# Kernel tuning notes

Hardware: AMD Instinct MI355X
Metric: run time of the kernel (lower is better)

## Reference

```python
import jax, jax.numpy as jnp
import numpy as np

H = 1024  # hidden_size == input_size


def setup_inputs() -> dict:
    key = jax.random.key(0)
    ks = jax.random.split(key, 12)
    B, T, S, I = 64, 128, 256, 1024
    sc_in = 1.0 / np.sqrt(I)
    sc_h = 1.0 / np.sqrt(H)
    return {
        "trg_emb": jax.random.normal(ks[0], (B, T, I), jnp.float32),
        "h0": jax.random.normal(ks[1], (B, H), jnp.float32),
        "c0": jax.random.normal(ks[2], (B, H), jnp.float32),
        "ctx": jax.random.normal(ks[3], (B, S, H), jnp.float32),
        "src_len": jax.random.randint(ks[4], (B,), 1, S + 1, jnp.int32),
        # nn.LSTM params (gate order i, f, g, o)
        "W_ih": jax.random.uniform(ks[5], (4 * H, I), jnp.float32, -sc_h, sc_h),
        "W_hh": jax.random.uniform(ks[6], (4 * H, H), jnp.float32, -sc_h, sc_h),
        "b_ih": jax.random.uniform(ks[7], (4 * H,), jnp.float32, -sc_h, sc_h),
        "b_hh": jax.random.uniform(ks[8], (4 * H,), jnp.float32, -sc_h, sc_h),
        # GlobalAttention (Luong general): linear_in (H->H), linear_out (2H->H), no bias
        "W_in": jax.random.uniform(ks[9], (H, H), jnp.float32, -sc_h, sc_h),
        "W_out": jax.random.uniform(ks[10], (H, 2 * H), jnp.float32, -sc_h, sc_h),
    }


def _lstm_scan(trg_emb, h0, c0, W_ih, W_hh, b_ih, b_hh):
    # Precompute input contributions for all steps: [B,T,4H] -> scan over T
    x_gates = jnp.einsum('bti,gi->btg', trg_emb, W_ih) + b_ih + b_hh

    def step(carry, xg):
        h, c = carry
        gates = xg + h @ W_hh.T  # [B,4H]
        i, f, g, o = jnp.split(gates, 4, axis=-1)
        c = jax.nn.sigmoid(f) * c + jax.nn.sigmoid(i) * jnp.tanh(g)
        h = jax.nn.sigmoid(o) * jnp.tanh(c)
        return (h, c), h

    (hT, cT), hs = jax.lax.scan(step, (h0, c0), jnp.swapaxes(x_gates, 0, 1))
    return jnp.swapaxes(hs, 0, 1), hT, cT  # [B,T,H], [B,H], [B,H]


def reference(trg_emb, h0, c0, ctx, src_len, W_ih, W_hh, b_ih, b_hh, W_in, W_out):
    # input_feed=False: LSTM recurrence is independent of attention -> run once,
    # then batch the global attention over all T timesteps (same math as the loop).
    lstm_out, hT, cT = _lstm_scan(trg_emb, h0, c0, W_ih, W_hh, b_ih, b_hh)

    q = jnp.einsum('bth,gh->btg', lstm_out, W_in)          # linear_in
    scores = jnp.einsum('bth,bsh->bts', q, ctx)            # [B,T,S]
    mask = jnp.arange(ctx.shape[1])[None, None, :] < src_len[:, None, None]
    scores = jnp.where(mask, scores, -jnp.inf)
    attn = jax.nn.softmax(scores, axis=-1)                 # att_dropout=0
    context = jnp.einsum('bts,bsh->bth', attn, ctx)        # [B,T,H]
    h_tilde = jnp.tanh(
        jnp.einsum('btc,hc->bth', jnp.concatenate([context, lstm_out], axis=-1), W_out)
    )  # [B,T,H]
    return h_tilde, (hT[None], cT[None])
```

## Files before the change

kernel.cpp:

```cpp
#include <hip/hip_runtime.h>
#include <math.h>

#define BB 64
#define TT 128
#define SS 256
#define HHH 1024

typedef unsigned short u16;
typedef unsigned int u32;
typedef unsigned long long u64t;
typedef __bf16 bf16x8 __attribute__((ext_vector_type(8)));
typedef float f32x4 __attribute__((ext_vector_type(4)));
typedef u16 u16x8 __attribute__((ext_vector_type(8)));

__device__ __forceinline__ float sigmoidf_(float x) { return 1.0f / (1.0f + expf(-x)); }
__device__ __forceinline__ u16 f2bf(float f) {
    __bf16 h = (__bf16)f;
    return __builtin_bit_cast(u16, h);
}
__device__ __forceinline__ float b2f(u16 u) {
    return __builtin_bit_cast(float, (u32)u << 16);
}
template <typename OT>
__device__ __forceinline__ void stout(OT* p, float v) {
    if constexpr (sizeof(OT) == 2) *p = f2bf(v); else *p = v;
}
__device__ __forceinline__ void astore(u64t* p, u64t v) {
    __hip_atomic_store(p, v, __ATOMIC_RELAXED, __HIP_MEMORY_SCOPE_AGENT);
}
__device__ __forceinline__ int afetchadd(int* p) {
    return __hip_atomic_fetch_add(p, 1, __ATOMIC_RELAXED, __HIP_MEMORY_SCOPE_AGENT);
}
__device__ __forceinline__ int aload32(const int* p) {
    return __hip_atomic_load(p, __ATOMIC_RELAXED, __HIP_MEMORY_SCOPE_AGENT);
}
__device__ __forceinline__ void astore32(int* p, int v) {
    __hip_atomic_store(p, v, __ATOMIC_RELAXED, __HIP_MEMORY_SCOPE_AGENT);
}
#define GLOAD16(gsrc, ldst)                                                      \
    __builtin_amdgcn_global_load_lds(                                            \
        (const __attribute__((address_space(1))) unsigned int*)(const void*)(gsrc), \
        (__attribute__((address_space(3))) unsigned int*)(void*)(ldst), 16, 0, 0)

__global__ __launch_bounds__(256) void convert_all(
    const float* __restrict__ trg, const float* __restrict__ wih,
    const float* __restrict__ win, const float* __restrict__ wout,
    u16* __restrict__ trg16, u16* __restrict__ wih16,
    u16* __restrict__ win16, u16* __restrict__ wout16)
{
    int b = blockIdx.x;
    const float* in;
    u16* out;
    long base;
    if (b < 4096)      { in = trg;  out = trg16;  base = (long)b * 2048; }
    else if (b < 6144) { in = wih;  out = wih16;  base = (long)(b - 4096) * 2048; }
    else if (b < 6656) { in = win;  out = win16;  base = (long)(b - 6144) * 2048; }
    else               { in = wout; out = wout16; base = (long)(b - 6656) * 2048; }
    long i = base + (long)threadIdx.x * 8;
    float4 a = *(const float4*)(in + i);
    float4 c = *(const float4*)(in + i + 4);
    u16x8 o;
    o[0] = f2bf(a.x); o[1] = f2bf(a.y); o[2] = f2bf(a.z); o[3] = f2bf(a.w);
    o[4] = f2bf(c.x); o[5] = f2bf(c.y); o[6] = f2bf(c.z); o[7] = f2bf(c.w);
    *(u16x8*)(out + i) = o;
}

__global__ __launch_bounds__(128) void wfrag_build(const float* __restrict__ W,
                                                   u16* __restrict__ WF) {
    const int w = blockIdx.x, kq = blockIdx.y, bid = blockIdx.z;
    const int t = threadIdx.x;
    const int rh = t >> 6, lane = t & 63;
    const int rowp = bid * 32 + rh * 16 + (lane & 15);
    const int g = rowp & 3, jrow = rowp >> 2;
    const int k = kq * 256 + w * 32 + (lane >> 4) * 8;
    const float* src = W + ((size_t)(g * 1024 + jrow) << 10) + k;
    float4 v0 = *(const float4*)src;
    float4 v1 = *(const float4*)(src + 4);
    float vv[8] = {v0.x, v0.y, v0.z, v0.w, v1.x, v1.y, v1.z, v1.w};
    u16x8 hi, lo;
#pragma unroll
    for (int i = 0; i < 8; ++i) {
        u16 h = f2bf(vv[i]);
        hi[i] = h;
        lo[i] = f2bf(vv[i] - b2f(h));
    }
    size_t fr = ((((size_t)bid * 4 + kq) * 8 + w) * 2 + rh) * 2;
    *(u16x8*)(WF + fr * 512 + (size_t)lane * 8) = hi;
    *(u16x8*)(WF + (fr + 1) * 512 + (size_t)lane * 8) = lo;
}

__global__ __launch_bounds__(256) void h0frag(const float* __restrict__ h0,
                                              u16* __restrict__ slot) {
    int i = blockIdx.x * 256 + threadIdx.x;
    int b = i >> 7, jg = i & 127;
    int j = jg << 3;
    const float* src = h0 + ((size_t)b << 10) + j;
    float4 v0 = *(const float4*)src;
    float4 v1 = *(const float4*)(src + 4);
    float vv[8] = {v0.x, v0.y, v0.z, v0.w, v1.x, v1.y, v1.z, v1.w};
    u16x8 hi, lo;
#pragma unroll
    for (int e = 0; e < 8; ++e) {
        u16 h = f2bf(vv[e]);
        hi[e] = h;
        lo[e] = f2bf(vv[e] - b2f(h));
    }
    int g = b >> 4, bl = b & 15;
    int kq = j >> 8, w = (j >> 5) & 7, tr = (j >> 3) & 3;
    int lane = tr * 16 + bl;
    size_t base = (size_t)g * 32768 + (size_t)((kq * 8 + w) * 2) * 512 + (size_t)lane * 8;
    *(u16x8*)(slot + base) = hi;
    *(u16x8*)(slot + base + 512) = lo;
}

template <bool TANH, bool AREMAP, bool BIAS, typename OT>
__global__ __launch_bounds__(256) void gemm_mfma_bt(
    const u16* __restrict__ A0, const u16* __restrict__ A1,
    const u16* __restrict__ B, OT* __restrict__ C,
    int M, int N, int K, int KA0,
    const float* __restrict__ bias0, const float* __restrict__ bias1)
{
    __shared__ uint4 As4[512];
    __shared__ uint4 Bs4[512];
    u16* As = (u16*)As4;
    u16* Bs = (u16*)Bs4;
    const int tid = threadIdx.x;
    const int l = tid & 63;
    const int w = tid >> 6;
    const int wm = w >> 1, wn = w & 1;
    const int tc = l & 15, tr8 = (l >> 4) << 3;
    const int m0 = blockIdx.y << 7, n0 = blockIdx.x << 7;
    f32x4 acc[4][4] = {};

    for (int k0 = 0; k0 < K; k0 += 32) {
        const u16* Ap = (k0 < KA0) ? A0 : A1;
        const int koff = (k0 < KA0) ? k0 : k0 - KA0;
#pragma unroll
        for (int r = 0; r < 2; ++r) {
            int u = tid + (r << 8);
            int row = u >> 2, q = u & 3;
            size_t arow;
            if (AREMAP) {
                int rr = m0 + row;
                arow = (size_t)((rr & 63) * 128 + (rr >> 6));
            } else {
                arow = (size_t)(m0 + row);
            }
            GLOAD16(Ap + arow * KA0 + koff + (q << 3), &As4[u]);
            GLOAD16(B + (size_t)(n0 + row) * K + k0 + (q << 3), &Bs4[u]);
        }
        __syncthreads();
        bf16x8 bfr[4];
#pragma unroll
        for (int j = 0; j < 4; ++j)
            bfr[j] = *(const bf16x8*)(Bs + ((wn << 6) + (j << 4) + tc) * 32 + tr8);
#pragma unroll
        for (int i = 0; i < 4; ++i) {
            bf16x8 af = *(const bf16x8*)(As + ((wm << 6) + (i << 4) + tc) * 32 + tr8);
#pragma unroll
            for (int j = 0; j < 4; ++j)
                acc[i][j] = __builtin_amdgcn_mfma_f32_16x16x32_bf16(af, bfr[j], acc[i][j], 0, 0, 0);
        }
        __syncthreads();
    }
#pragma unroll
    for (int j = 0; j < 4; ++j) {
        const int col = n0 + (wn << 6) + (j << 4) + tc;
        const float bias = BIAS ? (bias0[col] + bias1[col]) : 0.0f;
#pragma unroll
        for (int i = 0; i < 4; ++i) {
#pragma unroll
            for (int v = 0; v < 4; ++v) {
                int r = m0 + (wm << 6) + (i << 4) + ((l >> 4) << 2) + v;
                float val = acc[i][j][v] + bias;
                if (TANH) val = tanhf(val);
                stout(&C[(size_t)r * N + col], val);
            }
        }
    }
}

__global__ __launch_bounds__(512) void lstm_scan9(
    const float* __restrict__ xg, const u16* __restrict__ WF,
    const float* __restrict__ c0,
    const u16* __restrict__ h0s, u16* __restrict__ ring,
    float* __restrict__ hT, float* __restrict__ cT,
    u16* __restrict__ lstm16, int* __restrict__ bar)
{
    __shared__ float red[4][64][17];
    __shared__ __align__(8) u16 tileh[16][16];
    __shared__ __align__(8) u16 tilel[16][16];
    const int tid = threadIdx.x;
    const int bid = blockIdx.x;
    const int g = bid >> 6;
    const int ib = bid & 63;
    const int kg = tid >> 6, l = tid & 63;
    const int kq = kg & 3, rh = kg >> 2;
    const int j0 = ib << 4;
    const int ejl = tid & 15;
    const int ebl = (tid >> 4) & 15;

    bf16x8 wfh[2][8], wfl[2][8];
#pragma unroll
    for (int rt = 0; rt < 2; ++rt) {
        const int R16 = ib * 4 + rh * 2 + rt;
        const int bw = R16 >> 1, rhw = R16 & 1;
#pragma unroll
        for (int w = 0; w < 8; ++w) {
            size_t fr = ((((size_t)bw * 4 + kq) * 8 + w) * 2 + rhw) * 2;
            wfh[rt][w] = *(const bf16x8*)(WF + fr * 512 + (size_t)l * 8);
            wfl[rt][w] = *(const bf16x8*)(WF + (fr + 1) * 512 + (size_t)l * 8);
        }
    }
    float cv = 0.0f;
    if (tid < 256) cv = c0[(size_t)(g * 16 + ebl) * 1024 + j0 + ejl];

    float xgv[4] = {};
    if (tid < 256) {
#pragma unroll
        for (int g2 = 0; g2 < 4; ++g2)
            xgv[g2] = xg[(size_t)(g * 16 + ebl) * 4096 + (size_t)(g2 << 10) + j0 + ejl];
    }

    const int kqs = ib >> 4, ws = (ib >> 1) & 7;
    int* const gbar = bar + (g << 9);

    for (int t = 0; t < 128; ++t) {
        const u16* hin = ((t == 0) ? h0s : (ring + (size_t)(t - 1) * 131072)) + (size_t)g * 32768;
        u16* hout = ring + (size_t)t * 131072 + (size_t)g * 32768;

        f32x4 acc[2] = {};
        bf16x8 hbA[2], hbB[2];
#define LDW(HB, W)                                                                  \
        {                                                                           \
            size_t fb = (size_t)((kq * 8 + (W)) * 2) * 512 + (size_t)l * 8;         \
            HB[0] = *(const bf16x8*)(hin + fb);                                     \
            HB[1] = *(const bf16x8*)(hin + fb + 512);                               \
        }
        LDW(hbA, 0)
#pragma unroll
        for (int w = 0; w < 8; w += 2) {
            LDW(hbB, w + 1)
#pragma unroll
            for (int rt = 0; rt < 2; ++rt) {
                acc[rt] = __builtin_amdgcn_mfma_f32_16x16x32_bf16(wfh[rt][w], hbA[0], acc[rt], 0, 0, 0);
                acc[rt] = __builtin_amdgcn_mfma_f32_16x16x32_bf16(wfh[rt][w], hbA[1], acc[rt], 0, 0, 0);
                acc[rt] = __builtin_amdgcn_mfma_f32_16x16x32_bf16(wfl[rt][w], hbA[0], acc[rt], 0, 0, 0);
            }
            if (w + 2 < 8) LDW(hbA, w + 2)
#pragma unroll
            for (int rt = 0; rt < 2; ++rt) {
                acc[rt] = __builtin_amdgcn_mfma_f32_16x16x32_bf16(wfh[rt][w + 1], hbB[0], acc[rt], 0, 0, 0);
                acc[rt] = __builtin_amdgcn_mfma_f32_16x16x32_bf16(wfh[rt][w + 1], hbB[1], acc[rt], 0, 0, 0);
                acc[rt] = __builtin_amdgcn_mfma_f32_16x16x32_bf16(wfl[rt][w + 1], hbB[0], acc[rt], 0, 0, 0);
            }
        }
#undef LDW

#pragma unroll
        for (int rt = 0; rt < 2; ++rt)
#pragma unroll
            for (int v = 0; v < 4; ++v)
                red[kq][(rh << 5) + (rt << 4) + ((l >> 4) << 2) + v][l & 15] = acc[rt][v];
        __syncthreads();

        if (tid < 256) {
            float gate[4];
#pragma unroll
            for (int g2 = 0; g2 < 4; ++g2) {
                int rr = (ejl << 2) + g2;
                gate[g2] = red[0][rr][ebl] + red[1][rr][ebl] +
                           red[2][rr][ebl] + red[3][rr][ebl] + xgv[g2];
            }
            float ii = sigmoidf_(gate[0]);
            float ff = sigmoidf_(gate[1]);
            float gg = tanhf(gate[2]);
            float oo = sigmoidf_(gate[3]);
            float cn = ff * cv + ii * gg;
            float hn = oo * tanhf(cn);
            cv = cn;
            u16 hh = f2bf(hn);
            tileh[ebl][ejl] = hh;
            tilel[ebl][ejl] = f2bf(hn - b2f(hh));
            if (t == 127) {
                hT[(size_t)(g * 16 + ebl) * 1024 + j0 + ejl] = hn;
                cT[(size_t)(g * 16 + ebl) * 1024 + j0 + ejl] = cn;
            }
        }
        __syncthreads();

        if (tid < 128) {
            const int plane = tid >> 6, rem = tid & 63;
            const int b2 = rem >> 2, half = (rem >> 1) & 1, qq = rem & 1;
            const int lane = ((ib & 1) * 2 + half) * 16 + b2;
            const u16* tp = plane ? &tilel[b2][half * 8 + qq * 4] : &tileh[b2][half * 8 + qq * 4];
            size_t a16 = (size_t)(((kqs * 8 + ws) * 2 + plane)) * 512 + (size_t)lane * 8 + qq * 4;
            astore((u64t*)(hout + a16), *(const u64t*)tp);
            if (plane == 0) {
                int qj = rem & 3;
                *(u64t*)(lstm16 + ((size_t)(g * 16 + b2) * 128 + t) * 1024 + j0 + qj * 4) =
                    *(const u64t*)&tileh[b2][qj * 4];
            }
        }

        if (t < 127) {
            if (tid < 256) {
#pragma unroll
                for (int g2 = 0; g2 < 4; ++g2)
                    xgv[g2] = xg[(size_t)((t + 1) * 64 + g * 16 + ebl) * 4096 +
                                 (size_t)(g2 << 10) + j0 + ejl];
            }
            __syncthreads();
            if (tid == 0) {
                const int leaf = ib & 7;
                int a = afetchadd(&gbar[leaf * 16]);
                if ((a & 7) == 7) {
                    int r = afetchadd(&gbar[128]);
                    if ((r & 7) == 7) astore32(&gbar[136], t + 1);
                    while (aload32(&gbar[136]) < t + 1) __builtin_amdgcn_s_sleep(1);
                    astore32(&gbar[144 + leaf * 16], t + 1);
                } else {
                    while (aload32(&gbar[144 + leaf * 16]) < t + 1)
                        __builtin_amdgcn_s_sleep(1);
                }
            }
            __syncthreads();
        }
    }
}

__global__ __launch_bounds__(256) void scores_mfma(
    const float* __restrict__ q, const float* __restrict__ ctx,
    float* __restrict__ C)
{
    __shared__ u16 Ahi[4096], Alo[4096], Bhi[4096], Blo[4096];
    const int tid = threadIdx.x;
    const int l = tid & 63, w = tid >> 6;
    const int wm = w >> 1, wn = w & 1;
    const int tc = l & 15, tr8 = (l >> 4) << 3;
    const int b = blockIdx.z, n0 = blockIdx.x << 7;
    const float* A = q + (size_t)b * 131072;
    const float* B = ctx + (size_t)b * 262144;
    f32x4 acc[4][4] = {};

    for (int k0 = 0; k0 < 1024; k0 += 32) {
#pragma unroll
        for (int r = 0; r < 4; ++r) {
            int flat = r * 256 + tid;
            int row = flat >> 3, kq = (flat & 7) << 2;
            int o = row * 32 + kq;
            float4 va = *(const float4*)(A + (size_t)row * 1024 + k0 + kq);
            u16 a0 = f2bf(va.x), a1 = f2bf(va.y), a2 = f2bf(va.z), a3 = f2bf(va.w);
            *(ushort4*)&Ahi[o] = (ushort4){a0, a1, a2, a3};
            *(ushort4*)&Alo[o] = (ushort4){f2bf(va.x - b2f(a0)), f2bf(va.y - b2f(a1)),
                                           f2bf(va.z - b2f(a2)), f2bf(va.w - b2f(a3))};
            float4 vb = *(const float4*)(B + (size_t)(n0 + row) * 1024 + k0 + kq);
            u16 g0 = f2bf(vb.x), g1 = f2bf(vb.y), g2 = f2bf(vb.z), g3 = f2bf(vb.w);
            *(ushort4*)&Bhi[o] = (ushort4){g0, g1, g2, g3};
            *(ushort4*)&Blo[o] = (ushort4){f2bf(vb.x - b2f(g0)), f2bf(vb.y - b2f(g1)),
                                           f2bf(vb.z - b2f(g2)), f2bf(vb.w - b2f(g3))};
        }
        __syncthreads();
        bf16x8 bh[4], bl[4];
#pragma unroll
        for (int j = 0; j < 4; ++j) {
            int o = ((wn << 6) + (j << 4) + tc) * 32 + tr8;
            bh[j] = *(const bf16x8*)(Bhi + o);
            bl[j] = *(const bf16x8*)(Blo + o);
        }
#pragma unroll
        for (int i = 0; i < 4; ++i) {
            int o = ((wm << 6) + (i << 4) + tc) * 32 + tr8;
            bf16x8 ah = *(const bf16x8*)(Ahi + o);
            bf16x8 al = *(const bf16x8*)(Alo + o);
#pragma unroll
            for (int j = 0; j < 4; ++j) {
                acc[i][j] = __builtin_amdgcn_mfma_f32_16x16x32_bf16(ah, bh[j], acc[i][j], 0, 0, 0);
                acc[i][j] = __builtin_amdgcn_mfma_f32_16x16x32_bf16(ah, bl[j], acc[i][j], 0, 0, 0);
                acc[i][j] = __builtin_amdgcn_mfma_f32_16x16x32_bf16(al, bh[j], acc[i][j], 0, 0, 0);
            }
        }
        __syncthreads();
    }
#pragma unroll
    for (int j = 0; j < 4; ++j) {
        int col = n0 + (wn << 6) + (j << 4) + tc;
#pragma unroll
        for (int i = 0; i < 4; ++i)
#pragma unroll
            for (int v = 0; v < 4; ++v) {
                int r = (wm << 6) + (i << 4) + ((l >> 4) << 2) + v;
                C[(size_t)b * 32768 + (size_t)r * 256 + col] = acc[i][j][v];
            }
    }
}

__global__ __launch_bounds__(256) void softmax_mask16(
    const float* __restrict__ scores, const int* __restrict__ src_len,
    u16* __restrict__ attn16)
{
    __shared__ float red[4];
    const int b = blockIdx.y, t = blockIdx.x, s = threadIdx.x;
    const float* row = scores + ((long)b * TT + t) * SS;
    const int L = src_len[b];
    float v = (s < L) ? row[s] : -INFINITY;
    float m = v;
#pragma unroll
    for (int o = 32; o >= 1; o >>= 1) m = fmaxf(m, __shfl_xor(m, o));
    if ((s & 63) == 0) red[s >> 6] = m;
    __syncthreads();
    m = fmaxf(fmaxf(red[0], red[1]), fmaxf(red[2], red[3]));
    __syncthreads();
    float e = (s < L) ? expf(v - m) : 0.0f;
    float sum = e;
#pragma unroll
    for (int o = 32; o >= 1; o >>= 1) sum += __shfl_xor(sum, o);
    if ((s & 63) == 0) red[s >> 6] = sum;
    __syncthreads();
    sum = red[0] + red[1] + red[2] + red[3];
    attn16[((long)b * TT + t) * SS + s] = f2bf(e / sum);
}

__global__ __launch_bounds__(256) void ctxattn_mfma(
    const u16* __restrict__ attn16, const float* __restrict__ ctx,
    u16* __restrict__ ctxout16)
{
    __shared__ u16 As[4096];
    __shared__ u16 Bs[128][40];
    const int tid = threadIdx.x;
    const int l = tid & 63, w = tid >> 6;
    const int wm = w >> 1, wn = w & 1;
    const int tc = l & 15, tr8 = (l >> 4) << 3;
    const int b = blockIdx.z, n0 = blockIdx.x << 7;
    f32x4 acc[4][4] = {};

    for (int k0 = 0; k0 < 256; k0 += 32) {
        {
            int row = tid >> 1, off = (tid & 1) << 4;
            const u16* src = attn16 + (size_t)b * 32768 + (size_t)row * 256 + k0 + off;
            *(uint4*)&As[row * 32 + off] = *(const uint4*)src;
            *(uint4*)&As[row * 32 + off + 8] = *(const uint4*)(src + 8);
        }
#pragma unroll
        for (int p = 0; p < 4; ++p) {
            int flat = p * 256 + tid;
            int s = flat >> 5, hc = flat & 31;
            float4 v = *(const float4*)(ctx + (size_t)b * 262144 +
                                        (size_t)(k0 + s) * 1024 + n0 + (hc << 2));
            Bs[(hc << 2) + 0][s] = f2bf(v.x);
            Bs[(hc << 2) + 1][s] = f2bf(v.y);
            Bs[(hc << 2) + 2][s] = f2bf(v.z);
            Bs[(hc << 2) + 3][s] = f2bf(v.w);
        }
        __syncthreads();
        bf16x8 bfr[4];
#pragma unroll
        for (int j = 0; j < 4; ++j)
            bfr[j] = *(const bf16x8*)&Bs[(wn << 6) + (j << 4) + tc][tr8];
#pragma unroll
        for (int i = 0; i < 4; ++i) {
            bf16x8 af = *(const bf16x8*)(As + ((wm << 6) + (i << 4) + tc) * 32 + tr8);
#pragma unroll
            for (int j = 0; j < 4; ++j)
                acc[i][j] = __builtin_amdgcn_mfma_f32_16x16x32_bf16(af, bfr[j], acc[i][j], 0, 0, 0);
        }
        __syncthreads();
    }
#pragma unroll
    for (int j = 0; j < 4; ++j) {
        int col = n0 + (wn << 6) + (j << 4) + tc;
#pragma unroll
        for (int i = 0; i < 4; ++i)
#pragma unroll
            for (int v = 0; v < 4; ++v) {
                int r = (wm << 6) + (i << 4) + ((l >> 4) << 2) + v;
                ctxout16[((size_t)b * 128 + r) * 1024 + col] = f2bf(acc[i][j][v]);
            }
    }
}

extern "C" void kernel_launch(void* const* d_in, const int* in_sizes, int n_in,
                              void* d_out, int out_size, void* d_ws, size_t ws_size,
                              hipStream_t stream)
{
    const float* trg_emb = (const float*)d_in[0];
    const float* h0      = (const float*)d_in[1];
    const float* c0      = (const float*)d_in[2];
    const float* ctx     = (const float*)d_in[3];
    const int*   src_len = (const int*)d_in[4];
    const float* W_ih    = (const float*)d_in[5];
    const float* W_hh    = (const float*)d_in[6];
    const float* b_ih    = (const float*)d_in[7];
    const float* b_hh    = (const float*)d_in[8];
    const float* W_in    = (const float*)d_in[9];
    const float* W_out   = (const float*)d_in[10];

    float* out = (float*)d_out;
    float* h_tilde = out;
    float* hT = out + (size_t)BB * TT * HHH;
    float* cT = hT + (size_t)BB * HHH;

    char* w = (char*)d_ws;
    auto take = [&](size_t bytes) { void* p = w; w += (bytes + 255) & ~(size_t)255; return p; };
    char* base0 = w;
    u16* trg16  = (u16*)take(8388608ull * 2);
    u16* Wih16  = (u16*)take(4194304ull * 2);
    take(8388608ull);
    u16* ring   = (u16*)base0;
    u16* h0s    = (u16*)take(262144ull);
    u16* Win16  = (u16*)take(1048576ull * 2);
    u16* Wout16 = (u16*)take(2097152ull * 2);
    u16* lstm16 = (u16*)take(8388608ull * 2);
    u16* WF     = (u16*)take(16777216ull);
    int* bar    = (int*)take(8192);
    char* regionB = w;
    float* xg = (float*)take(33554432ull * 4);
    float* q        = (float*)regionB;
    float* scores   = (float*)(regionB + 33554432ull);
    u16*   attn16   = (u16*)(regionB + 41943040ull);
    u16*   ctxout16 = (u16*)(regionB + 46137344ull);

    hipMemsetAsync(bar, 0, 8192, stream);

    convert_all<<<7680, 256, 0, stream>>>(trg_emb, W_ih, W_in, W_out,
                                          trg16, Wih16, Win16, Wout16);
    wfrag_build<<<dim3(8, 4, 128), 128, 0, stream>>>(W_hh, WF);
    h0frag<<<32, 256, 0, stream>>>(h0, h0s);

    gemm_mfma_bt<false, true, true, float><<<dim3(32, 64), 256, 0, stream>>>(
        trg16, trg16, Wih16, xg, 8192, 4096, 1024, 1024, b_ih, b_hh);

    lstm_scan9<<<256, 512, 0, stream>>>(xg, WF, c0, h0s, ring,
                                        hT, cT, lstm16, bar);

    gemm_mfma_bt<false, false, false, float><<<dim3(8, 64), 256, 0, stream>>>(
        lstm16, lstm16, Win16, q, 8192, 1024, 1024, 1024, nullptr, nullptr);

    scores_mfma<<<dim3(2, 1, 64), 256, 0, stream>>>(q, ctx, scores);

    softmax_mask16<<<dim3(TT, BB, 1), 256, 0, stream>>>(scores, src_len, attn16);

    ctxattn_mfma<<<dim3(8, 1, 64), 256, 0, stream>>>(attn16, ctx, ctxout16);

    gemm_mfma_bt<true, false, false, float><<<dim3(8, 64), 256, 0, stream>>>(
        ctxout16, lstm16, Wout16, h_tilde, 8192, 1024, 2048, 1024, nullptr, nullptr);
}
```

Baseline: 1.026 ms.

## Transpose xg layout for coalesced LSTM loads and prefetch next step early

The input-gate GEMM now writes its output in a per-timestep, gate-interleaved, batch-minor layout, so each LSTM block's gate loads are contiguous across batch lanes. The thread mapping in the scan swaps batch and hidden indices to match. The next step's gate inputs are loaded at the start of the current step instead of just before the grid barrier, which hides their latency behind the MFMA work. The cost is a scattered, less coalesced epilogue store in the GEMM and extra registers for the double buffer.

```diff
diff --git a/kernel.cpp b/kernel.cpp
--- a/kernel.cpp
+++ b/kernel.cpp
@@ -113,7 +113,7 @@
     *(u16x8*)(slot + base + 512) = lo;
 }
 
-template <bool TANH, bool AREMAP, bool BIAS, typename OT>
+template <bool TANH, bool XGT, typename OT>
 __global__ __launch_bounds__(256) void gemm_mfma_bt(
     const u16* __restrict__ A0, const u16* __restrict__ A1,
     const u16* __restrict__ B, OT* __restrict__ C,
@@ -140,7 +140,7 @@
             int u = tid + (r << 8);
             int row = u >> 2, q = u & 3;
             size_t arow;
-            if (AREMAP) {
+            if (XGT) {
                 int rr = m0 + row;
                 arow = (size_t)((rr & 63) * 128 + (rr >> 6));
             } else {
@@ -166,22 +166,27 @@
 #pragma unroll
     for (int j = 0; j < 4; ++j) {
         const int col = n0 + (wn << 6) + (j << 4) + tc;
-        const float bias = BIAS ? (bias0[col] + bias1[col]) : 0.0f;
+        const float bias = XGT ? (bias0[col] + bias1[col]) : 0.0f;
 #pragma unroll
         for (int i = 0; i < 4; ++i) {
 #pragma unroll
             for (int v = 0; v < 4; ++v) {
                 int r = m0 + (wm << 6) + (i << 4) + ((l >> 4) << 2) + v;
-                float val = acc[i][j][v] + bias;
-                if (TANH) val = tanhf(val);
-                stout(&C[(size_t)r * N + col], val);
-            }
-        }
-    }
-}
-
-__global__ __launch_bounds__(512) void lstm_scan9(
-    const float* __restrict__ xg, const u16* __restrict__ WF,
+                float val = acc[i][j][v];
+                if (XGT) {
+                    int newr = ((col & 1023) << 2) | (col >> 10);
+                    ((float*)C)[(size_t)(r >> 6) * 262144 + (size_t)newr * 64 + (r & 63)] = val + bias;
+                } else {
+                    if (TANH) val = tanhf(val);
+                    stout(&C[(size_t)r * N + col], val);
+                }
+            }
+        }
+    }
+}
+
+__global__ __launch_bounds__(512) void lstm_scan10(
+    const float* __restrict__ xgt, const u16* __restrict__ WF,
     const float* __restrict__ c0,
     const u16* __restrict__ h0s, u16* __restrict__ ring,
     float* __restrict__ hT, float* __restrict__ cT,
@@ -197,8 +202,8 @@
     const int kg = tid >> 6, l = tid & 63;
     const int kq = kg & 3, rh = kg >> 2;
     const int j0 = ib << 4;
-    const int ejl = tid & 15;
-    const int ebl = (tid >> 4) & 15;
+    const int ebl = tid & 15;
+    const int ejl = (tid >> 4) & 15;
 
     bf16x8 wfh[2][8], wfl[2][8];
 #pragma unroll
@@ -215,11 +220,11 @@
     float cv = 0.0f;
     if (tid < 256) cv = c0[(size_t)(g * 16 + ebl) * 1024 + j0 + ejl];
 
-    float xgv[4] = {};
+    float xgvA[4] = {}, xgvB[4] = {};
     if (tid < 256) {
 #pragma unroll
         for (int g2 = 0; g2 < 4; ++g2)
-            xgv[g2] = xg[(size_t)(g * 16 + ebl) * 4096 + (size_t)(g2 << 10) + j0 + ejl];
+            xgvA[g2] = xgt[(size_t)(((j0 + ejl) << 2) + g2) * 64 + g * 16 + ebl];
     }
 
     const int kqs = ib >> 4, ws = (ib >> 1) & 7;
@@ -228,6 +233,13 @@
     for (int t = 0; t < 128; ++t) {
         const u16* hin = ((t == 0) ? h0s : (ring + (size_t)(t - 1) * 131072)) + (size_t)g * 32768;
         u16* hout = ring + (size_t)t * 131072 + (size_t)g * 32768;
+
+        if (t < 127 && tid < 256) {
+#pragma unroll
+            for (int g2 = 0; g2 < 4; ++g2)
+                xgvB[g2] = xgt[(size_t)(t + 1) * 262144 +
+                               (size_t)(((j0 + ejl) << 2) + g2) * 64 + g * 16 + ebl];
+        }
 
         f32x4 acc[2] = {};
         bf16x8 hbA[2], hbB[2];
@@ -270,7 +282,7 @@
             for (int g2 = 0; g2 < 4; ++g2) {
                 int rr = (ejl << 2) + g2;
                 gate[g2] = red[0][rr][ebl] + red[1][rr][ebl] +
-                           red[2][rr][ebl] + red[3][rr][ebl] + xgv[g2];
+                           red[2][rr][ebl] + red[3][rr][ebl] + xgvA[g2];
             }
             float ii = sigmoidf_(gate[0]);
             float ff = sigmoidf_(gate[1]);
@@ -304,12 +316,6 @@
         }
 
         if (t < 127) {
-            if (tid < 256) {
-#pragma unroll
-                for (int g2 = 0; g2 < 4; ++g2)
-                    xgv[g2] = xg[(size_t)((t + 1) * 64 + g * 16 + ebl) * 4096 +
-                                 (size_t)(g2 << 10) + j0 + ejl];
-            }
             __syncthreads();
             if (tid == 0) {
                 const int leaf = ib & 7;
@@ -325,6 +331,8 @@
                 }
             }
             __syncthreads();
+#pragma unroll
+            for (int g2 = 0; g2 < 4; ++g2) xgvA[g2] = xgvB[g2];
         }
     }
 }
@@ -514,7 +522,7 @@
     u16* WF     = (u16*)take(16777216ull);
     int* bar    = (int*)take(8192);
     char* regionB = w;
-    float* xg = (float*)take(33554432ull * 4);
+    float* xgt = (float*)take(33554432ull * 4);
     float* q        = (float*)regionB;
     float* scores   = (float*)(regionB + 33554432ull);
     u16*   attn16   = (u16*)(regionB + 41943040ull);
@@ -527,13 +535,13 @@
     wfrag_build<<<dim3(8, 4, 128), 128, 0, stream>>>(W_hh, WF);
     h0frag<<<32, 256, 0, stream>>>(h0, h0s);
 
-    gemm_mfma_bt<false, true, true, float><<<dim3(32, 64), 256, 0, stream>>>(
-        trg16, trg16, Wih16, xg, 8192, 4096, 1024, 1024, b_ih, b_hh);
-
-    lstm_scan9<<<256, 512, 0, stream>>>(xg, WF, c0, h0s, ring,
-                                        hT, cT, lstm16, bar);
-
-    gemm_mfma_bt<false, false, false, float><<<dim3(8, 64), 256, 0, stream>>>(
+    gemm_mfma_bt<false, true, float><<<dim3(32, 64), 256, 0, stream>>>(
+        trg16, trg16, Wih16, xgt, 8192, 4096, 1024, 1024, b_ih, b_hh);
+
+    lstm_scan10<<<256, 512, 0, stream>>>(xgt, WF, c0, h0s, ring,
+                                         hT, cT, lstm16, bar);
+
+    gemm_mfma_bt<false, false, float><<<dim3(8, 64), 256, 0, stream>>>(
         lstm16, lstm16, Win16, q, 8192, 1024, 1024, 1024, nullptr, nullptr);
 
     scores_mfma<<<dim3(2, 1, 64), 256, 0, stream>>>(q, ctx, scores);
@@ -542,6 +550,6 @@
 
     ctxattn_mfma<<<dim3(8, 1, 64), 256, 0, stream>>>(attn16, ctx, ctxout16);
 
-    gemm_mfma_bt<true, false, false, float><<<dim3(8, 64), 256, 0, stream>>>(
+    gemm_mfma_bt<true, false, float><<<dim3(8, 64), 256, 0, stream>>>(
         ctxout16, lstm16, Wout16, h_tilde, 8192, 1024, 2048, 1024, nullptr, nullptr);
 }
```

Measured after the change: 1.015 ms. No clear change (-1.1%).
